# Kernel tuning notes

Hardware: AMD Instinct MI355X
Metric: run time of the kernel (lower is better)

Reference implementation:

```python
import jax, jax.numpy as jnp
import numpy as np

B, S, E, H = 2, 2048, 1024, 16
D = E // H  # head_dim = 64


def setup_inputs() -> dict:
    key = jax.random.key(0)
    ks = jax.random.split(key, 9)
    s = 1.0 / np.sqrt(E)
    return {
        "x": jax.random.normal(ks[0], (B, S, E), dtype=jnp.float32),
        "Wq": jax.random.uniform(ks[1], (E, E), jnp.float32, -s, s),
        "bq": jax.random.uniform(ks[2], (E,), jnp.float32, -s, s),
        "Wk": jax.random.uniform(ks[3], (E, E), jnp.float32, -s, s),
        "bk": jax.random.uniform(ks[4], (E,), jnp.float32, -s, s),
        "Wv": jax.random.uniform(ks[5], (E, E), jnp.float32, -s, s),
        "bv": jax.random.uniform(ks[6], (E,), jnp.float32, -s, s),
        "Wo": jax.random.uniform(ks[7], (E, E), jnp.float32, -s, s),
        "bo": jax.random.uniform(ks[8], (E,), jnp.float32, -s, s),
    }


def reference(x, Wq, bq, Wk, bk, Wv, bv, Wo, bo):
    # QKV projections (torch Linear: x @ W.T + b), split into heads: [B,H,S,D]
    def proj(t, W, b):
        return (t @ W.T + b).reshape(B, S, H, D).transpose(0, 2, 1, 3)

    Q = proj(x, Wq, bq)
    K = proj(x, Wk, bk)
    V = proj(x, Wv, bv)
    # scores [B,H,S,S], scaled by sqrt(head_dim)
    score = jnp.einsum('bnqd,bnkd->bnqk', Q, K) / jnp.sqrt(jnp.float32(D))
    weights = jax.nn.softmax(score, axis=-1)
    out = jnp.einsum('bnql,bnld->bnqd', weights, V)  # [B,H,S,D]
    out = out.transpose(0, 2, 1, 3).reshape(B, S, E)
    return out @ Wo.T + bo
```

## Files before the change

kernel.cpp:

```cpp
#include <hip/hip_runtime.h>


#define B_ 2
#define S_ 2048
#define E_ 1024
#define H_ 16
#define D_ 64
#define M_ (B_ * S_)

typedef __attribute__((ext_vector_type(8))) _Float16 f16x8;
typedef __attribute__((ext_vector_type(4))) _Float16 f16x4;
typedef __attribute__((ext_vector_type(2))) _Float16 f16x2;
typedef __attribute__((ext_vector_type(4))) float f32x4;
typedef __attribute__((ext_vector_type(16))) float f32x16;
typedef __attribute__((ext_vector_type(8))) unsigned short u16x8;
typedef __attribute__((ext_vector_type(4))) unsigned int u32x4;

#define LOG2E  1.44269504f
#define CLOG2  4.32808512f

#define KROW 144
#define KBUF 9216
#define VBASE 18432
#define SMEMSZ 36864

static __device__ __forceinline__ float bf16_to_f32(unsigned short u) {
    return __uint_as_float(((unsigned)u) << 16);
}
static __device__ __forceinline__ unsigned short f32_to_bf16(float f) {
    unsigned u = __float_as_uint(f);
    u += 0x7FFFu + ((u >> 16) & 1u);
    return (unsigned short)(u >> 16);
}
static __device__ __forceinline__ float load1_f32(const void* p, int i, bool isbf) {
    return isbf ? bf16_to_f32(((const unsigned short*)p)[i]) : ((const float*)p)[i];
}
static __device__ __forceinline__ void store1(void* p, size_t i, float v, bool isbf) {
    if (isbf) ((unsigned short*)p)[i] = f32_to_bf16(v);
    else      ((float*)p)[i] = v;
}
static __device__ __forceinline__ void gl2lds16(const void* g, void* l) {
    __builtin_amdgcn_global_load_lds((const __attribute__((address_space(1))) unsigned int*)g,
                                     (__attribute__((address_space(3))) unsigned int*)l, 16, 0, 0);
}
static __device__ __forceinline__ float rexp2(float x) {
    float r;
    asm("v_exp_f32 %0, %1" : "=v"(r) : "v"(x));
    return r;
}
static __device__ __forceinline__ unsigned pk2(float a, float b) {
    return __builtin_bit_cast(unsigned, __builtin_amdgcn_cvt_pkrtz(a, b));
}

__global__ __launch_bounds__(256) void convert_inputs(
    const void* __restrict__ x,  const void* __restrict__ wq,
    const void* __restrict__ wk, const void* __restrict__ wv,
    const void* __restrict__ wo,
    _Float16* __restrict__ x16, _Float16* __restrict__ w16,
    int* __restrict__ flag_out)
{
    __shared__ int sflag;
    const int tid = threadIdx.x;
    if (tid < 64) {
        const unsigned short hh = ((const unsigned short*)x)[2 * tid];
        const int e = (hh >> 7) & 0xFF;
        const bool sane = (e >= 0x60 && e <= 0x9F);
        const unsigned long long m = __ballot(sane);
        if (tid == 0) sflag = (__popcll(m) >= 48) ? 1 : 0;
    }
    __syncthreads();
    const bool isbf = sflag != 0;
    if (blockIdx.x == 0 && tid == 0) *flag_out = sflag;

    const size_t t = ((size_t)blockIdx.x * 256 + tid) * 8;
    const void* src; size_t off; _Float16* dst; float scale = 1.0f;
    if (t < (size_t)M_ * E_) { src = x; off = t; dst = x16 + t; }
    else {
        const size_t u = t - (size_t)M_ * E_;
        const int wsel = (int)(u >> 20);
        off = u & ((1u << 20) - 1);
        src = wsel == 0 ? wq : wsel == 1 ? wk : wsel == 2 ? wv : wo;
        dst = w16 + u;
        if (wsel == 0) scale = 0.125f * LOG2E;
    }
    f16x8 v;
    if (isbf) {
        u16x8 s = *(const u16x8*)((const unsigned short*)src + off);
        #pragma unroll
        for (int j = 0; j < 8; ++j) v[j] = (_Float16)(bf16_to_f32(s[j]) * scale);
    } else {
        const float* f = (const float*)src + off;
        f32x4 lo = *(const f32x4*)f;
        f32x4 hi = *(const f32x4*)(f + 4);
        #pragma unroll
        for (int j = 0; j < 4; ++j) {
            v[j]     = (_Float16)(lo[j] * scale);
            v[4 + j] = (_Float16)(hi[j] * scale);
        }
    }
    *(f16x8*)dst = v;
}

__global__ __launch_bounds__(256) void gemm_qkv(
    const _Float16* __restrict__ x16, const _Float16* __restrict__ w16,
    const void* __restrict__ bq, const void* __restrict__ bk, const void* __restrict__ bv,
    const int* __restrict__ flag,
    _Float16* __restrict__ Qb, _Float16* __restrict__ Kb, _Float16* __restrict__ VTb)
{
    __shared__ __align__(16) _Float16 As[128 * 64];
    __shared__ __align__(16) _Float16 Bs[128 * 64];
    const bool isbf = (*flag != 0);
    const int tid = threadIdx.x, wave = tid >> 6, lane = tid & 63;
    const int wm = wave >> 1, wn = wave & 1;
    const int qd = lane >> 4, ln = lane & 15;
    const int m0 = blockIdx.x * 128;
    const int by = blockIdx.y;
    const int wsel = by >> 3;
    const int n0 = (by & 7) * 128;
    const _Float16* W = w16 + ((size_t)wsel << 20);

    char* dX = (wsel == 2) ? (char*)Bs : (char*)As;
    char* dW = (wsel == 2) ? (char*)As : (char*)Bs;

    const _Float16* gx[4]; const _Float16* gw[4];
    char* lx[4]; char* lw[4];
    #pragma unroll
    for (int it = 0; it < 4; ++it) {
        const int seg = it * 256 + tid;
        const int row = seg >> 3, cg = seg & 7;
        const int scol = ((cg + row) & 7) * 8;
        gx[it] = x16 + (size_t)(m0 + row) * E_ + scol;
        gw[it] = W + (size_t)(n0 + row) * E_ + scol;
        lx[it] = dX + (size_t)(it * 256 + wave * 64) * 16;
        lw[it] = dW + (size_t)(it * 256 + wave * 64) * 16;
    }

    const int sw0 = ((qd - ln) & 7) * 8;
    const int sw1 = ((qd + 4 - ln) & 7) * 8;

    f32x4 acc[16] = {};

    for (int kt = 0; kt < E_; kt += 64) {
        __syncthreads();
        #pragma unroll
        for (int it = 0; it < 4; ++it) {
            gl2lds16(gx[it] + kt, lx[it]);
            gl2lds16(gw[it] + kt, lw[it]);
        }
        __syncthreads();
        #pragma unroll
        for (int kk = 0; kk < 2; ++kk) {
            const int sw = kk ? sw1 : sw0;
            f16x8 a[4], bfr[4];
            #pragma unroll
            for (int mt = 0; mt < 4; ++mt)
                a[mt] = *(const f16x8*)&As[((wm * 64 + mt * 16 + ln) << 6) + sw];
            #pragma unroll
            for (int nt = 0; nt < 4; ++nt)
                bfr[nt] = *(const f16x8*)&Bs[((wn * 64 + nt * 16 + ln) << 6) + sw];
            #pragma unroll
            for (int mt = 0; mt < 4; ++mt)
                #pragma unroll
                for (int nt = 0; nt < 4; ++nt)
                    acc[mt * 4 + nt] = __builtin_amdgcn_mfma_f32_16x16x32_f16(a[mt], bfr[nt], acc[mt * 4 + nt], 0, 0, 0);
        }
    }

    if (wsel != 2) {
        const void* bias = wsel == 0 ? bq : bk;
        const float bscale = (wsel == 0) ? 0.125f * LOG2E : 1.0f;
        _Float16* dst = wsel == 0 ? Qb : Kb;
        #pragma unroll
        for (int nt = 0; nt < 4; ++nt) {
            const int n = n0 + wn * 64 + nt * 16 + ln;
            const float bvv = load1_f32(bias, n, isbf) * bscale;
            const int h = n >> 6, d = n & 63;
            #pragma unroll
            for (int mt = 0; mt < 4; ++mt)
                #pragma unroll
                for (int r = 0; r < 4; ++r) {
                    const int m = m0 + wm * 64 + mt * 16 + qd * 4 + r;
                    const int b = m >> 11, s = m & (S_ - 1);
                    dst[((size_t)(b * H_ + h) * S_ + s) * D_ + d] =
                        (_Float16)(acc[mt * 4 + nt][r] + bvv);
                }
        }
    } else {
        #pragma unroll
        for (int mt = 0; mt < 4; ++mt)
            #pragma unroll
            for (int r = 0; r < 4; ++r) {
                const int e = n0 + wm * 64 + mt * 16 + qd * 4 + r;
                const float bvv = load1_f32(bv, e, isbf);
                const int h = e >> 6, d = e & 63;
                #pragma unroll
                for (int nt = 0; nt < 4; ++nt) {
                    const int sg = m0 + wn * 64 + nt * 16 + ln;
                    const int b = sg >> 11, s = sg & (S_ - 1);
                    VTb[((size_t)(b * H_ + h) * D_ + d) * S_ + s] =
                        (_Float16)(acc[mt * 4 + nt][r] + bvv);
                }
            }
    }
}

__global__ __launch_bounds__(256, 4) void attn(
    const _Float16* __restrict__ Q, const _Float16* __restrict__ K,
    const _Float16* __restrict__ VT, _Float16* __restrict__ AO)
{
    __shared__ __align__(16) char smem[SMEMSZ];

    const int tid = threadIdx.x, wave = tid >> 6, lane = tid & 63;
    const int rl = lane & 31, h = lane >> 5;
    const int qg = wave & 1, kh = wave >> 1;
    const int L = blockIdx.x;
    const int bh = ((L & 7) << 2) | ((L >> 3) & 3);
    const int qt = L >> 5;
    const int b = bh >> 4, hh = bh & (H_ - 1);

    const _Float16* Kbase = K + (size_t)bh * S_ * D_;
    const _Float16* Vbase = VT + (size_t)bh * D_ * S_;

    f16x8 qf[4];
    {
        const _Float16* qrow = Q + ((size_t)bh * S_ + qt * 64 + qg * 32 + rl) * D_ + h * 8;
        #pragma unroll
        for (int c = 0; c < 4; ++c) qf[c] = *(const f16x8*)(qrow + c * 16);
    }

    f16x8 ones;
    #pragma unroll
    for (int j = 0; j < 8; ++j) ones[j] = (_Float16)1.0f;

    const _Float16* kg[2]; const _Float16* vg[2]; int sw[2];
    #pragma unroll
    for (int it = 0; it < 2; ++it) {
        const int seg = it * 256 + tid;
        const int row = seg >> 3, c = seg & 7;
        kg[it] = Kbase + (size_t)row * D_ + c * 8;
        vg[it] = Vbase + (size_t)row * S_ + c * 8;
        sw[it] = row * KROW + c * 16;
    }

    int koff[4];
    #pragma unroll
    for (int c = 0; c < 4; ++c)
        koff[c] = (kh * 32 + rl) * KROW + (((c << 1) | h) << 4);
    const int vrow0 = rl * KROW, vrow1 = (32 + rl) * KROW;
    const int vka = kh * 64 + h * 8;

    f32x16 o0 = {}, o1 = {}, li = {};

    {
        f16x8 kr[2], vr[2];
        #pragma unroll
        for (int it = 0; it < 2; ++it) { kr[it] = *(const f16x8*)kg[it]; vr[it] = *(const f16x8*)vg[it]; }
        #pragma unroll
        for (int it = 0; it < 2; ++it) {
            *(f16x8*)(smem + sw[it])         = kr[it];
            *(f16x8*)(smem + VBASE + sw[it]) = vr[it];
        }
    }
    __syncthreads();

    for (int kt = 0; kt < S_; kt += 64) {
        const int p = (kt >> 6) & 1;
        const bool more = (kt + 64) < S_;

        f16x8 kr[2], vr[2];
        if (more) {
            #pragma unroll
            for (int it = 0; it < 2; ++it) {
                kr[it] = *(const f16x8*)(kg[it] + (size_t)(kt + 64) * D_);
                vr[it] = *(const f16x8*)(vg[it] + (kt + 64));
            }
        }

        const char* kb = smem + p * KBUF;
        const char* vb = smem + VBASE + p * KBUF;

        f16x8 af[4];
        #pragma unroll
        for (int c = 0; c < 4; ++c) af[c] = *(const f16x8*)(kb + koff[c]);

        f32x16 sc = {};
        __builtin_amdgcn_s_setprio(1);
        #pragma unroll
        for (int c = 0; c < 4; ++c)
            sc = __builtin_amdgcn_mfma_f32_32x32x16_f16(af[c], qf[c], sc, 0, 0, 0);
        __builtin_amdgcn_s_setprio(0);

        float e[16];
        #pragma unroll
        for (int i = 0; i < 16; ++i) e[i] = rexp2(sc[i] - CLOG2);

        #pragma unroll
        for (int ks = 0; ks < 2; ++ks) {
            const int oo = 8 * ks;
            const f16x8 pf = __builtin_bit_cast(f16x8, (u32x4){
                pk2(e[oo + 0], e[oo + 1]), pk2(e[oo + 2], e[oo + 3]),
                pk2(e[oo + 4], e[oo + 5]), pk2(e[oo + 6], e[oo + 7])});

            const int cA = vka + ks * 32;
            const f16x4 a0 = *(const f16x4*)(vb + vrow0 + cA);
            const f16x4 b0 = *(const f16x4*)(vb + vrow0 + cA + 16);
            const f16x4 a1 = *(const f16x4*)(vb + vrow1 + cA);
            const f16x4 b1 = *(const f16x4*)(vb + vrow1 + cA + 16);
            const f16x8 v0 = __builtin_shufflevector(a0, b0, 0, 1, 2, 3, 4, 5, 6, 7);
            const f16x8 v1 = __builtin_shufflevector(a1, b1, 0, 1, 2, 3, 4, 5, 6, 7);

            __builtin_amdgcn_s_setprio(1);
            o0 = __builtin_amdgcn_mfma_f32_32x32x16_f16(pf, v0, o0, 0, 0, 0);
            o1 = __builtin_amdgcn_mfma_f32_32x32x16_f16(pf, v1, o1, 0, 0, 0);
            li = __builtin_amdgcn_mfma_f32_32x32x16_f16(pf, ones, li, 0, 0, 0);
            __builtin_amdgcn_s_setprio(0);
        }

        if (more) {
            #pragma unroll
            for (int it = 0; it < 2; ++it) {
                *(f16x8*)(smem + (p ^ 1) * KBUF + sw[it])         = kr[it];
                *(f16x8*)(smem + VBASE + (p ^ 1) * KBUF + sw[it]) = vr[it];
            }
        }
        __syncthreads();
    }

    float* red = (float*)smem;
    const int rbase = qg * 64 + lane;
    if (kh) {
        #pragma unroll
        for (int i = 0; i < 16; ++i) {
            red[i * 128 + rbase]        = o0[i];
            red[(16 + i) * 128 + rbase] = o1[i];
            red[(32 + i) * 128 + rbase] = li[i];
        }
    }
    __syncthreads();
    if (!kh) {
        #pragma unroll
        for (int i = 0; i < 16; ++i) {
            const float t0 = o0[i] + red[i * 128 + rbase];
            const float t1 = o1[i] + red[(16 + i) * 128 + rbase];
            const float tl = li[i] + red[(32 + i) * 128 + rbase];
            const float inv = 1.0f / tl;
            const int q = qt * 64 + qg * 32 + 4 * h + (i & 3) + 8 * (i >> 2);
            _Float16* dst = AO + ((size_t)b * S_ + q) * E_ + hh * D_;
            dst[rl]      = (_Float16)(t0 * inv);
            dst[32 + rl] = (_Float16)(t1 * inv);
        }
    }
}

__global__ __launch_bounds__(256) void gemm_out(
    const _Float16* __restrict__ A, const _Float16* __restrict__ W,
    const void* __restrict__ bias, const int* __restrict__ flag, void* __restrict__ out)
{
    __shared__ __align__(16) _Float16 As[128 * 64];
    __shared__ __align__(16) _Float16 Bs[64 * 64];
    const bool isbf = (*flag != 0);
    const int tid = threadIdx.x, wave = tid >> 6, lane = tid & 63;
    const int wm = wave >> 1, wn = wave & 1;
    const int qd = lane >> 4, ln = lane & 15;
    const int m0 = blockIdx.x * 128;
    const int n0 = blockIdx.y * 64;

    const _Float16* ga[4]; char* la[4];
    #pragma unroll
    for (int it = 0; it < 4; ++it) {
        const int seg = it * 256 + tid;
        const int row = seg >> 3, cg = seg & 7;
        const int scol = ((cg + row) & 7) * 8;
        ga[it] = A + (size_t)(m0 + row) * E_ + scol;
        la[it] = (char*)As + (size_t)(it * 256 + wave * 64) * 16;
    }
    const _Float16* gb[2]; char* lb[2];
    #pragma unroll
    for (int it = 0; it < 2; ++it) {
        const int seg = it * 256 + tid;
        const int row = seg >> 3, cg = seg & 7;
        const int scol = ((cg + row) & 7) * 8;
        gb[it] = W + (size_t)(n0 + row) * E_ + scol;
        lb[it] = (char*)Bs + (size_t)(it * 256 + wave * 64) * 16;
    }
    const int sw0 = ((qd - ln) & 7) * 8;
    const int sw1 = ((qd + 4 - ln) & 7) * 8;

    f32x4 acc[8] = {};

    for (int kt = 0; kt < E_; kt += 64) {
        __syncthreads();
        #pragma unroll
        for (int it = 0; it < 4; ++it) gl2lds16(ga[it] + kt, la[it]);
        #pragma unroll
        for (int it = 0; it < 2; ++it) gl2lds16(gb[it] + kt, lb[it]);
        __syncthreads();
        #pragma unroll
        for (int kk = 0; kk < 2; ++kk) {
            const int sw = kk ? sw1 : sw0;
            f16x8 a[4], bfr[2];
            #pragma unroll
            for (int mt = 0; mt < 4; ++mt)
                a[mt] = *(const f16x8*)&As[((wm * 64 + mt * 16 + ln) << 6) + sw];
            #pragma unroll
            for (int nt = 0; nt < 2; ++nt)
                bfr[nt] = *(const f16x8*)&Bs[((wn * 32 + nt * 16 + ln) << 6) + sw];
            #pragma unroll
            for (int mt = 0; mt < 4; ++mt)
                #pragma unroll
                for (int nt = 0; nt < 2; ++nt)
                    acc[mt * 2 + nt] = __builtin_amdgcn_mfma_f32_16x16x32_f16(a[mt], bfr[nt], acc[mt * 2 + nt], 0, 0, 0);
        }
    }

    #pragma unroll
    for (int nt = 0; nt < 2; ++nt) {
        const int n = n0 + wn * 32 + nt * 16 + ln;
        const float bvv = load1_f32(bias, n, isbf);
        #pragma unroll
        for (int mt = 0; mt < 4; ++mt)
            #pragma unroll
            for (int r = 0; r < 4; ++r) {
                const int m = m0 + wm * 64 + mt * 16 + qd * 4 + r;
                store1(out, (size_t)m * E_ + n, acc[mt * 2 + nt][r] + bvv, isbf);
            }
    }
}

extern "C" void kernel_launch(void* const* d_in, const int* in_sizes, int n_in,
                              void* d_out, int out_size, void* d_ws, size_t ws_size,
                              hipStream_t stream) {
    const void* x  = d_in[0];
    const void* Wq = d_in[1];
    const void* bq = d_in[2];
    const void* Wk = d_in[3];
    const void* bk = d_in[4];
    const void* Wv = d_in[5];
    const void* bv = d_in[6];
    const void* Wo = d_in[7];
    const void* bo = d_in[8];

    int* flag = (int*)d_ws;
    _Float16* x16 = (_Float16*)((char*)d_ws + 1024);
    _Float16* w16 = x16 + (size_t)M_ * E_;
    _Float16* Qb  = w16 + 4u * (size_t)E_ * E_;
    _Float16* Kb  = Qb + (size_t)M_ * E_;
    _Float16* VTb = Kb + (size_t)M_ * E_;
    _Float16* AO  = x16;

    convert_inputs<<<4096, 256, 0, stream>>>(x, Wq, Wk, Wv, Wo, x16, w16, flag);
    gemm_qkv<<<dim3(32, 24), 256, 0, stream>>>(x16, w16, bq, bk, bv, flag, Qb, Kb, VTb);
    attn<<<1024, 256, 0, stream>>>(Qb, Kb, VTb, AO);
    gemm_out<<<dim3(32, 16), 256, 0, stream>>>(AO, w16 + 3u * (size_t)E_ * E_, bo, flag, d_out);
}
```

Before: 199.5 us.

## Replace row-sum MFMA with scalar lane sums and re-layout V smem for 16B reads

Removes the third MFMA per k-step that multiplied P by a ones vector to get softmax denominators. Each lane now sums its 16 exp values in registers, and the partial sums go through shared memory at the end. The V tile is also stored in shared memory with a permuted column layout, so each PV operand is one 16-byte LDS read instead of two 8-byte reads plus a shuffle. The cost is extra VALU adds, split 8-byte LDS stores on V writes, and reliance on the score accumulator mapping each lane's outputs to a single query row.

```diff
diff --git a/kernel.cpp b/kernel.cpp
--- a/kernel.cpp
+++ b/kernel.cpp
@@ -228,18 +228,15 @@
         for (int c = 0; c < 4; ++c) qf[c] = *(const f16x8*)(qrow + c * 16);
     }
 
-    f16x8 ones;
-    #pragma unroll
-    for (int j = 0; j < 8; ++j) ones[j] = (_Float16)1.0f;
-
-    const _Float16* kg[2]; const _Float16* vg[2]; int sw[2];
+    const _Float16* kg[2]; const _Float16* vg[2]; int swk[2], swv[2];
     #pragma unroll
     for (int it = 0; it < 2; ++it) {
         const int seg = it * 256 + tid;
         const int row = seg >> 3, c = seg & 7;
         kg[it] = Kbase + (size_t)row * D_ + c * 8;
         vg[it] = Vbase + (size_t)row * S_ + c * 8;
-        sw[it] = row * KROW + c * 16;
+        swk[it] = row * KROW + c * 16;
+        swv[it] = row * KROW + (c >> 1) * 32 + (c & 1) * 8;
     }
 
     int koff[4];
@@ -247,9 +244,10 @@
     for (int c = 0; c < 4; ++c)
         koff[c] = (kh * 32 + rl) * KROW + (((c << 1) | h) << 4);
     const int vrow0 = rl * KROW, vrow1 = (32 + rl) * KROW;
-    const int vka = kh * 64 + h * 8;
-
-    f32x16 o0 = {}, o1 = {}, li = {};
+    const int vcol = h * 16;
+
+    f32x16 o0 = {}, o1 = {};
+    float lisum = 0.0f;
 
     {
         f16x8 kr[2], vr[2];
@@ -257,8 +255,9 @@
         for (int it = 0; it < 2; ++it) { kr[it] = *(const f16x8*)kg[it]; vr[it] = *(const f16x8*)vg[it]; }
         #pragma unroll
         for (int it = 0; it < 2; ++it) {
-            *(f16x8*)(smem + sw[it])         = kr[it];
-            *(f16x8*)(smem + VBASE + sw[it]) = vr[it];
+            *(f16x8*)(smem + swk[it]) = kr[it];
+            *(f16x4*)(smem + VBASE + swv[it])      = __builtin_shufflevector(vr[it], vr[it], 0, 1, 2, 3);
+            *(f16x4*)(smem + VBASE + swv[it] + 16) = __builtin_shufflevector(vr[it], vr[it], 4, 5, 6, 7);
         }
     }
     __syncthreads();
@@ -293,6 +292,9 @@
         float e[16];
         #pragma unroll
         for (int i = 0; i < 16; ++i) e[i] = rexp2(sc[i] - CLOG2);
+
+        lisum += (((e[0] + e[1]) + (e[2] + e[3])) + ((e[4] + e[5]) + (e[6] + e[7])))
+               + (((e[8] + e[9]) + (e[10] + e[11])) + ((e[12] + e[13]) + (e[14] + e[15])));
 
         #pragma unroll
         for (int ks = 0; ks < 2; ++ks) {
@@ -301,39 +303,36 @@
                 pk2(e[oo + 0], e[oo + 1]), pk2(e[oo + 2], e[oo + 3]),
                 pk2(e[oo + 4], e[oo + 5]), pk2(e[oo + 6], e[oo + 7])});
 
-            const int cA = vka + ks * 32;
-            const f16x4 a0 = *(const f16x4*)(vb + vrow0 + cA);
-            const f16x4 b0 = *(const f16x4*)(vb + vrow0 + cA + 16);
-            const f16x4 a1 = *(const f16x4*)(vb + vrow1 + cA);
-            const f16x4 b1 = *(const f16x4*)(vb + vrow1 + cA + 16);
-            const f16x8 v0 = __builtin_shufflevector(a0, b0, 0, 1, 2, 3, 4, 5, 6, 7);
-            const f16x8 v1 = __builtin_shufflevector(a1, b1, 0, 1, 2, 3, 4, 5, 6, 7);
+            const int go = ((kh * 2 + ks) << 5) + vcol;
+            const f16x8 v0 = *(const f16x8*)(vb + vrow0 + go);
+            const f16x8 v1 = *(const f16x8*)(vb + vrow1 + go);
 
             __builtin_amdgcn_s_setprio(1);
             o0 = __builtin_amdgcn_mfma_f32_32x32x16_f16(pf, v0, o0, 0, 0, 0);
             o1 = __builtin_amdgcn_mfma_f32_32x32x16_f16(pf, v1, o1, 0, 0, 0);
-            li = __builtin_amdgcn_mfma_f32_32x32x16_f16(pf, ones, li, 0, 0, 0);
             __builtin_amdgcn_s_setprio(0);
         }
 
         if (more) {
             #pragma unroll
             for (int it = 0; it < 2; ++it) {
-                *(f16x8*)(smem + (p ^ 1) * KBUF + sw[it])         = kr[it];
-                *(f16x8*)(smem + VBASE + (p ^ 1) * KBUF + sw[it]) = vr[it];
+                *(f16x8*)(smem + (p ^ 1) * KBUF + swk[it]) = kr[it];
+                *(f16x4*)(smem + VBASE + (p ^ 1) * KBUF + swv[it])      = __builtin_shufflevector(vr[it], vr[it], 0, 1, 2, 3);
+                *(f16x4*)(smem + VBASE + (p ^ 1) * KBUF + swv[it] + 16) = __builtin_shufflevector(vr[it], vr[it], 4, 5, 6, 7);
             }
         }
         __syncthreads();
     }
 
     float* red = (float*)smem;
+    float* lig = (float*)(smem + 16384);
     const int rbase = qg * 64 + lane;
+    lig[(qg * 32 + rl) * 4 + kh * 2 + h] = lisum;
     if (kh) {
         #pragma unroll
         for (int i = 0; i < 16; ++i) {
             red[i * 128 + rbase]        = o0[i];
             red[(16 + i) * 128 + rbase] = o1[i];
-            red[(32 + i) * 128 + rbase] = li[i];
         }
     }
     __syncthreads();
@@ -342,9 +341,10 @@
         for (int i = 0; i < 16; ++i) {
             const float t0 = o0[i] + red[i * 128 + rbase];
             const float t1 = o1[i] + red[(16 + i) * 128 + rbase];
-            const float tl = li[i] + red[(32 + i) * 128 + rbase];
-            const float inv = 1.0f / tl;
-            const int q = qt * 64 + qg * 32 + 4 * h + (i & 3) + 8 * (i >> 2);
+            const int ql = qg * 32 + 4 * h + (i & 3) + 8 * (i >> 2);
+            const f32x4 lv = *(const f32x4*)&lig[ql * 4];
+            const float inv = 1.0f / ((lv[0] + lv[1]) + (lv[2] + lv[3]));
+            const int q = qt * 64 + ql;
             _Float16* dst = AO + ((size_t)b * S_ + q) * E_ + hh * D_;
             dst[rl]      = (_Float16)(t0 * inv);
             dst[32 + rl] = (_Float16)(t1 * inv);
```

Result: no change. 196.8 us (-1.4%).
